# Kernel optimization log

Measured on AMD Instinct MI355X. Metric: run time of the kernel, lower is better.

## Reference

```python
import jax, jax.numpy as jnp
import numpy as np

NUM_HEADS = 8
WINDOW_SIZE = 4
DIM = 384


def setup_inputs() -> dict:
    key = jax.random.key(0)
    k_x, k_qkv, k_pw, k_pb = jax.random.split(key, 4)
    B, N, C = 8, 16384, DIM
    x = jax.random.normal(k_x, (B, N, C), dtype=jnp.float32)
    # torch nn.Linear weights are [out_features, in_features]
    W_qkv = jax.random.normal(k_qkv, (3 * C, C), dtype=jnp.float32) * (1.0 / np.sqrt(C))
    W_proj = jax.random.normal(k_pw, (C, C), dtype=jnp.float32) * (1.0 / np.sqrt(C))
    b_proj = jax.random.normal(k_pb, (C,), dtype=jnp.float32) * 0.01
    return {"x": x, "W_qkv": W_qkv, "W_proj": W_proj, "b_proj": b_proj}


def reference(x, W_qkv, W_proj, b_proj):
    B, N, C = x.shape
    H = int(round(N ** 0.5))
    W = H
    ws = WINDOW_SIZE
    nh = NUM_HEADS
    hd = C // nh
    scale = hd ** -0.5
    hw, ww = H // ws, W // ws

    qkv = x @ W_qkv.T  # [B, N, 3C]
    qkv = qkv.reshape(B, N, 3, nh, hd)
    qkv = jnp.transpose(qkv, (2, 0, 3, 1, 4))  # [3, B, nh, N, hd]
    q, k, v = qkv[0], qkv[1], qkv[2]

    def to_windows(t):
        # [B, nh, N, hd] -> [B, nh, n_windows, ws*ws, hd]
        t = t.reshape(B, nh, hw, ws, ww, ws, hd)
        t = jnp.transpose(t, (0, 1, 2, 4, 3, 5, 6))
        return t.reshape(B, nh, hw * ww, ws * ws, hd)

    q, k, v = to_windows(q), to_windows(k), to_windows(v)

    attn = jnp.einsum('bhwqd,bhwkd->bhwqk', q, k) * scale
    attn = jax.nn.softmax(attn, axis=-1)
    out = jnp.einsum('bhwqk,bhwkd->bhwqd', attn, v)

    # windows back to [B, N, C]
    out = out.reshape(B, nh, hw, ww, ws, ws, hd)
    out = jnp.transpose(out, (0, 1, 2, 4, 3, 5, 6)).reshape(B, nh, N, hd)
    out = jnp.transpose(out, (0, 2, 1, 3)).reshape(B, N, C)

    out = out @ W_proj.T + b_proj
    return out
```

## Files before the change

### kernel.cpp

```cpp
#include <hip/hip_runtime.h>
#include <hip/hip_bf16.h>
#include <cstdint>

#define ASPACE(n) __attribute__((address_space(n)))

typedef short bf16x8 __attribute__((ext_vector_type(8)));
typedef float f32x4 __attribute__((ext_vector_type(4)));

__device__ __forceinline__ unsigned short f2bf(float f) {
  uint32_t u = __float_as_uint(f);
  u += 0x7fffu + ((u >> 16) & 1u);
  return (unsigned short)(u >> 16);
}
__device__ __forceinline__ float bf2f(unsigned short h) {
  return __uint_as_float(((uint32_t)h) << 16);
}

__global__ __launch_bounds__(256) void conv_f32_bf16(const float4* __restrict__ src,
                                                     ushort4* __restrict__ dst, int n4) {
  int i = blockIdx.x * blockDim.x + threadIdx.x;
  int stride = gridDim.x * blockDim.x;
  for (; i < n4; i += stride) {
    float4 v = src[i];
    ushort4 o;
    o.x = f2bf(v.x); o.y = f2bf(v.y); o.z = f2bf(v.z); o.w = f2bf(v.w);
    dst[i] = o;
  }
}

__device__ __forceinline__ void gload16(const unsigned short* g, unsigned short* l) {
  __builtin_amdgcn_global_load_lds((const ASPACE(1) void*)g, (ASPACE(3) void*)l, 16, 0, 0);
}

template <int OUT_MODE>
__global__ __launch_bounds__(256, 3) void gemm_bt(const unsigned short* __restrict__ A,
                                                  const unsigned short* __restrict__ B,
                                                  void* __restrict__ Cout,
                                                  const float* __restrict__ bias,
                                                  int M, int N, int K) {
  __shared__ unsigned short As[2][128 * 32];
  __shared__ unsigned short Bs[2][192 * 32];

  const int tid  = threadIdx.x;
  const int lane = tid & 63;
  const int wave = tid >> 6;
  const int wr = wave >> 1;
  const int wc = wave & 1;

  const int nwg = gridDim.x;
  const int swz = (blockIdx.x & 7) * (nwg >> 3) + (blockIdx.x >> 3);
  const int ntn = N / 192;
  const int bn0 = (swz % ntn) * 192;
  const int bm0 = (swz / ntn) << 7;

  const unsigned short* Abase = A + (size_t)bm0 * K;
  const unsigned short* Bbase = B + (size_t)bn0 * K;

  const unsigned short* gA[2];
  const unsigned short* gB[3];
  unsigned short* lA[2];
  unsigned short* lB[3];
#pragma unroll
  for (int i = 0; i < 2; ++i) {
    const int c = i * 256 + tid;
    const int r = c >> 2;
    const int gc = (c & 3) ^ ((r >> 1) & 3);
    gA[i] = Abase + (size_t)r * K + gc * 8;
    lA[i] = (unsigned short*)As + (i * 256 + wave * 64) * 8;
  }
#pragma unroll
  for (int i = 0; i < 3; ++i) {
    const int c = i * 256 + tid;
    const int r = c >> 2;
    const int gc = (c & 3) ^ ((r >> 1) & 3);
    gB[i] = Bbase + (size_t)r * K + gc * 8;
    lB[i] = (unsigned short*)Bs + (i * 256 + wave * 64) * 8;
  }
  const int abufoff = 128 * 32;
  const int bbufoff = 192 * 32;

  const int fr = lane & 15;
  const int hi = lane >> 4;
  int afo[4], bfo[6];
#pragma unroll
  for (int m = 0; m < 4; ++m) {
    const int row = wr * 64 + m * 16 + fr;
    afo[m] = row * 32 + ((hi ^ ((row >> 1) & 3)) * 8);
  }
#pragma unroll
  for (int n = 0; n < 6; ++n) {
    const int row = wc * 96 + n * 16 + fr;
    bfo[n] = row * 32 + ((hi ^ ((row >> 1) & 3)) * 8);
  }

  f32x4 acc[4][6];
#pragma unroll
  for (int m = 0; m < 4; ++m)
#pragma unroll
    for (int n = 0; n < 6; ++n) {
      f32x4 z = {0.f, 0.f, 0.f, 0.f};
      acc[m][n] = z;
    }

  const int NT = K >> 5;

#pragma unroll
  for (int i = 0; i < 2; ++i) gload16(gA[i], lA[i]);
#pragma unroll
  for (int i = 0; i < 3; ++i) gload16(gB[i], lB[i]);
  __syncthreads();

  int cur = 0;
  for (int t = 0; t < NT; ++t) {
    if (t + 1 < NT) {
      const int nb = cur ^ 1;
      const int k0 = (t + 1) << 5;
#pragma unroll
      for (int i = 0; i < 2; ++i) gload16(gA[i] + k0, lA[i] + nb * abufoff);
#pragma unroll
      for (int i = 0; i < 3; ++i) gload16(gB[i] + k0, lB[i] + nb * bbufoff);
    }
    {
      const unsigned short* Ab = (const unsigned short*)As + cur * abufoff;
      const unsigned short* Bb = (const unsigned short*)Bs + cur * bbufoff;
      bf16x8 af[4], bfv[6];
#pragma unroll
      for (int m = 0; m < 4; ++m) af[m] = *(const bf16x8*)(Ab + afo[m]);
#pragma unroll
      for (int n = 0; n < 6; ++n) bfv[n] = *(const bf16x8*)(Bb + bfo[n]);
#pragma unroll
      for (int m = 0; m < 4; ++m)
#pragma unroll
        for (int n = 0; n < 6; ++n)
          acc[m][n] = __builtin_amdgcn_mfma_f32_16x16x32_bf16(af[m], bfv[n], acc[m][n], 0, 0, 0);
    }
    __syncthreads();
    cur ^= 1;
  }

  const int rq = hi * 4;
  if (OUT_MODE == 1) {
    float* C = (float*)Cout;
#pragma unroll
    for (int m = 0; m < 4; ++m) {
#pragma unroll
      for (int n = 0; n < 6; ++n) {
        const int col = bn0 + wc * 96 + n * 16 + fr;
        const float bv = bias[col];
#pragma unroll
        for (int r = 0; r < 4; ++r) {
          const int row = bm0 + wr * 64 + m * 16 + rq + r;
          C[(size_t)row * N + col] = acc[m][n][r] + bv;
        }
      }
    }
  } else {
    unsigned short* C = (unsigned short*)Cout;
#pragma unroll
    for (int m = 0; m < 4; ++m) {
#pragma unroll
      for (int n = 0; n < 6; ++n) {
        const int col = bn0 + wc * 96 + n * 16 + fr;
        const int pl = col / 48;
        const int d  = col - pl * 48;
        unsigned short* base = C + ((size_t)pl * M + bm0 + wr * 64 + m * 16 + rq) * 48 + d;
#pragma unroll
        for (int r = 0; r < 4; ++r)
          base[(size_t)r * 48] = f2bf(acc[m][n][r]);
      }
    }
  }
}

#define PADV 24
#define PADP 24
#define MTOK 131072
__global__ __launch_bounds__(256) void win_attn(const unsigned short* __restrict__ qkv,
                                                unsigned short* __restrict__ aout) {
  __shared__ unsigned short lds[4][48 * PADV + 16 * PADP];
  const int tid = threadIdx.x;
  const int wave = tid >> 6, lane = tid & 63;
  const int wg = blockIdx.x * 4 + wave;
  const int h = wg & 7;
  const int bw = wg >> 3;
  const int w = bw & 1023, b = bw >> 10;
  const int wy = w >> 5, wx = w & 31;

  unsigned short* Vt = lds[wave];
  unsigned short* P  = lds[wave] + 48 * PADV;

  const int lg = lane >> 4;
  const int lr = lane & 15;

  const int gtok = b * 16384 + (wy * 4 + (lr >> 2)) * 128 + wx * 4 + (lr & 3);
  const size_t qb = ((size_t)h * MTOK + gtok) * 48;
  const size_t kb = ((size_t)(8 + h) * MTOK + gtok) * 48;
  const size_t vb = ((size_t)(16 + h) * MTOK + gtok) * 48;

  bf16x8 aq0, bk0;
  bf16x8 aq1 = {0, 0, 0, 0, 0, 0, 0, 0};
  bf16x8 bk1 = {0, 0, 0, 0, 0, 0, 0, 0};
  aq0 = *(const bf16x8*)(qkv + qb + lg * 8);
  bk0 = *(const bf16x8*)(qkv + kb + lg * 8);
  if (lg < 2) {
    aq1 = *(const bf16x8*)(qkv + qb + 32 + lg * 8);
    bk1 = *(const bf16x8*)(qkv + kb + 32 + lg * 8);
  }

  {
    bf16x8 v = *(const bf16x8*)(qkv + vb + lg * 8);
#pragma unroll
    for (int i = 0; i < 8; ++i) Vt[(lg * 8 + i) * PADV + lr] = (unsigned short)v[i];
    if (lane < 32) {
      bf16x8 v2 = *(const bf16x8*)(qkv + vb + 32 + lg * 8);
#pragma unroll
      for (int i = 0; i < 8; ++i) Vt[((4 + lg) * 8 + i) * PADV + lr] = (unsigned short)v2[i];
    }
  }

  f32x4 s = {0.f, 0.f, 0.f, 0.f};
  s = __builtin_amdgcn_mfma_f32_16x16x32_bf16(aq0, bk0, s, 0, 0, 0);
  s = __builtin_amdgcn_mfma_f32_16x16x32_bf16(aq1, bk1, s, 0, 0, 0);

  const float scale = 0.14433756729740643f;
  float p[4];
#pragma unroll
  for (int r = 0; r < 4; ++r) {
    float x = s[r] * scale;
    float m = x;
    m = fmaxf(m, __shfl_xor(m, 1));
    m = fmaxf(m, __shfl_xor(m, 2));
    m = fmaxf(m, __shfl_xor(m, 4));
    m = fmaxf(m, __shfl_xor(m, 8));
    float e = __expf(x - m);
    float t = e;
    t += __shfl_xor(t, 1);
    t += __shfl_xor(t, 2);
    t += __shfl_xor(t, 4);
    t += __shfl_xor(t, 8);
    p[r] = e / t;
  }
#pragma unroll
  for (int r = 0; r < 4; ++r) P[(lg * 4 + r) * PADP + lr] = f2bf(p[r]);

  __syncthreads();

  bf16x8 ap = {0, 0, 0, 0, 0, 0, 0, 0};
  if (lg < 2) ap = *(const bf16x8*)(P + lr * PADP + lg * 8);

  f32x4 o[3];
#pragma unroll
  for (int c = 0; c < 3; ++c) {
    bf16x8 bv = {0, 0, 0, 0, 0, 0, 0, 0};
    if (lg < 2) bv = *(const bf16x8*)(Vt + (c * 16 + lr) * PADV + lg * 8);
    f32x4 z = {0.f, 0.f, 0.f, 0.f};
    o[c] = __builtin_amdgcn_mfma_f32_16x16x32_bf16(ap, bv, z, 0, 0, 0);
  }

#pragma unroll
  for (int r = 0; r < 4; ++r) {
    const int qi = lg * 4 + r;
    const int nq = (wy * 4 + (qi >> 2)) * 128 + wx * 4 + (qi & 3);
    const size_t obase = ((size_t)(b * 16384 + nq)) * 384 + h * 48;
#pragma unroll
    for (int c = 0; c < 3; ++c)
      aout[obase + c * 16 + lr] = f2bf(o[c][r]);
  }
}

extern "C" void kernel_launch(void* const* d_in, const int* in_sizes, int n_in,
                              void* d_out, int out_size, void* d_ws, size_t ws_size,
                              hipStream_t stream) {
  const float* x      = (const float*)d_in[0];
  const float* W_qkv  = (const float*)d_in[1];
  const float* W_proj = (const float*)d_in[2];
  const float* b_proj = (const float*)d_in[3];
  float* out = (float*)d_out;

  const int Bb = 8, Nn = 16384, Cc = 384;
  const int M = Bb * Nn;
  const int threeC = 3 * Cc;

  char* ws = (char*)d_ws;
  unsigned short* qkv_bf   = (unsigned short*)ws;
  unsigned short* xa_bf    = (unsigned short*)(ws + (size_t)M * threeC * 2);
  unsigned short* wqkv_bf  = (unsigned short*)(ws + (size_t)M * threeC * 2 + (size_t)M * Cc * 2);
  unsigned short* wproj_bf = wqkv_bf + threeC * Cc;

  conv_f32_bf16<<<2048, 256, 0, stream>>>((const float4*)x, (ushort4*)xa_bf, M * Cc / 4);
  conv_f32_bf16<<<432, 256, 0, stream>>>((const float4*)W_qkv, (ushort4*)wqkv_bf, threeC * Cc / 4);
  conv_f32_bf16<<<144, 256, 0, stream>>>((const float4*)W_proj, (ushort4*)wproj_bf, Cc * Cc / 4);

  gemm_bt<0><<<(M / 128) * (threeC / 192), 256, 0, stream>>>(xa_bf, wqkv_bf, qkv_bf, nullptr,
                                                             M, threeC, Cc);

  win_attn<<<Bb * 8 * 1024 / 4, 256, 0, stream>>>(qkv_bf, xa_bf);

  gemm_bt<1><<<(M / 128) * (Cc / 192), 256, 0, stream>>>(xa_bf, wproj_bf, out, b_proj,
                                                         M, Cc, Cc);
}
```

Before: 421.9 us.

## Fuse window attention with output projection GEMM via LDS-resident attention tile

```diff
diff --git a/kernel.cpp b/kernel.cpp
--- a/kernel.cpp
+++ b/kernel.cpp
@@ -32,12 +32,10 @@
   __builtin_amdgcn_global_load_lds((const ASPACE(1) void*)g, (ASPACE(3) void*)l, 16, 0, 0);
 }
 
-template <int OUT_MODE>
-__global__ __launch_bounds__(256, 3) void gemm_bt(const unsigned short* __restrict__ A,
-                                                  const unsigned short* __restrict__ B,
-                                                  void* __restrict__ Cout,
-                                                  const float* __restrict__ bias,
-                                                  int M, int N, int K) {
+__global__ __launch_bounds__(256, 3) void gemm_qkv(const unsigned short* __restrict__ A,
+                                                   const unsigned short* __restrict__ B,
+                                                   unsigned short* __restrict__ C,
+                                                   int M, int N, int K) {
   __shared__ unsigned short As[2][128 * 32];
   __shared__ unsigned short Bs[2][192 * 32];
 
@@ -139,132 +137,203 @@
   }
 
   const int rq = hi * 4;
-  if (OUT_MODE == 1) {
-    float* C = (float*)Cout;
-#pragma unroll
-    for (int m = 0; m < 4; ++m) {
-#pragma unroll
-      for (int n = 0; n < 6; ++n) {
-        const int col = bn0 + wc * 96 + n * 16 + fr;
-        const float bv = bias[col];
-#pragma unroll
-        for (int r = 0; r < 4; ++r) {
-          const int row = bm0 + wr * 64 + m * 16 + rq + r;
-          C[(size_t)row * N + col] = acc[m][n][r] + bv;
-        }
-      }
-    }
-  } else {
-    unsigned short* C = (unsigned short*)Cout;
-#pragma unroll
-    for (int m = 0; m < 4; ++m) {
-#pragma unroll
-      for (int n = 0; n < 6; ++n) {
-        const int col = bn0 + wc * 96 + n * 16 + fr;
-        const int pl = col / 48;
-        const int d  = col - pl * 48;
-        unsigned short* base = C + ((size_t)pl * M + bm0 + wr * 64 + m * 16 + rq) * 48 + d;
-#pragma unroll
-        for (int r = 0; r < 4; ++r)
-          base[(size_t)r * 48] = f2bf(acc[m][n][r]);
-      }
-    }
-  }
-}
-
-#define PADV 24
-#define PADP 24
+#pragma unroll
+  for (int m = 0; m < 4; ++m) {
+#pragma unroll
+    for (int n = 0; n < 6; ++n) {
+      const int col = bn0 + wc * 96 + n * 16 + fr;
+      const int pl = col / 48;
+      const int d  = col - pl * 48;
+      unsigned short* base = C + ((size_t)pl * M + bm0 + wr * 64 + m * 16 + rq) * 48 + d;
+#pragma unroll
+      for (int r = 0; r < 4; ++r)
+        base[(size_t)r * 48] = f2bf(acc[m][n][r]);
+    }
+  }
+}
+
 #define MTOK 131072
-__global__ __launch_bounds__(256) void win_attn(const unsigned short* __restrict__ qkv,
-                                                unsigned short* __restrict__ aout) {
-  __shared__ unsigned short lds[4][48 * PADV + 16 * PADP];
-  const int tid = threadIdx.x;
-  const int wave = tid >> 6, lane = tid & 63;
-  const int wg = blockIdx.x * 4 + wave;
-  const int h = wg & 7;
-  const int bw = wg >> 3;
-  const int w = bw & 1023, b = bw >> 10;
-  const int wy = w >> 5, wx = w & 31;
-
-  unsigned short* Vt = lds[wave];
-  unsigned short* P  = lds[wave] + 48 * PADV;
+#define ASTR 392
+__global__ __launch_bounds__(512, 2) void fused_attn_proj(const unsigned short* __restrict__ qkv,
+                                                          const unsigned short* __restrict__ Wp,
+                                                          const float* __restrict__ bias,
+                                                          float* __restrict__ out) {
+  __shared__ unsigned short lds[50176 + 24576];
+  unsigned short* attn = lds;
+  unsigned short* BsS  = lds + 50176;
+
+  const int tid = threadIdx.x, lane = tid & 63, wave = tid >> 6;
+  const int nwg = gridDim.x;
+  const int swz = (blockIdx.x & 7) * (nwg >> 3) + (blockIdx.x >> 3);
+  const int b = swz >> 7, g2 = swz & 127;
+  const int yb = g2 >> 2, xb = g2 & 3;
+  const int imgbase = b * 16384;
 
   const int lg = lane >> 4;
   const int lr = lane & 15;
 
-  const int gtok = b * 16384 + (wy * 4 + (lr >> 2)) * 128 + wx * 4 + (lr & 3);
-  const size_t qb = ((size_t)h * MTOK + gtok) * 48;
-  const size_t kb = ((size_t)(8 + h) * MTOK + gtok) * 48;
-  const size_t vb = ((size_t)(16 + h) * MTOK + gtok) * 48;
-
-  bf16x8 aq0, bk0;
-  bf16x8 aq1 = {0, 0, 0, 0, 0, 0, 0, 0};
-  bf16x8 bk1 = {0, 0, 0, 0, 0, 0, 0, 0};
-  aq0 = *(const bf16x8*)(qkv + qb + lg * 8);
-  bk0 = *(const bf16x8*)(qkv + kb + lg * 8);
-  if (lg < 2) {
-    aq1 = *(const bf16x8*)(qkv + qb + 32 + lg * 8);
-    bk1 = *(const bf16x8*)(qkv + kb + 32 + lg * 8);
-  }
-
   {
-    bf16x8 v = *(const bf16x8*)(qkv + vb + lg * 8);
-#pragma unroll
-    for (int i = 0; i < 8; ++i) Vt[(lg * 8 + i) * PADV + lr] = (unsigned short)v[i];
-    if (lane < 32) {
-      bf16x8 v2 = *(const bf16x8*)(qkv + vb + 32 + lg * 8);
-#pragma unroll
-      for (int i = 0; i < 8; ++i) Vt[((4 + lg) * 8 + i) * PADV + lr] = (unsigned short)v2[i];
-    }
-  }
-
-  f32x4 s = {0.f, 0.f, 0.f, 0.f};
-  s = __builtin_amdgcn_mfma_f32_16x16x32_bf16(aq0, bk0, s, 0, 0, 0);
-  s = __builtin_amdgcn_mfma_f32_16x16x32_bf16(aq1, bk1, s, 0, 0, 0);
-
-  const float scale = 0.14433756729740643f;
-  float p[4];
-#pragma unroll
-  for (int r = 0; r < 4; ++r) {
-    float x = s[r] * scale;
-    float m = x;
-    m = fmaxf(m, __shfl_xor(m, 1));
-    m = fmaxf(m, __shfl_xor(m, 2));
-    m = fmaxf(m, __shfl_xor(m, 4));
-    m = fmaxf(m, __shfl_xor(m, 8));
-    float e = __expf(x - m);
-    float t = e;
-    t += __shfl_xor(t, 1);
-    t += __shfl_xor(t, 2);
-    t += __shfl_xor(t, 4);
-    t += __shfl_xor(t, 8);
-    p[r] = e / t;
-  }
-#pragma unroll
-  for (int r = 0; r < 4; ++r) P[(lg * 4 + r) * PADP + lr] = f2bf(p[r]);
-
+    unsigned short* Vt = BsS + wave * 1536;
+    unsigned short* P  = Vt + 48 * 24;
+    const int gtok = imgbase + (yb * 4 + (lr >> 2)) * 128 + xb * 32 + wave * 4 + (lr & 3);
+
+    for (int h = 0; h < 8; ++h) {
+      const size_t qb = ((size_t)h * MTOK + gtok) * 48;
+      const size_t kb = ((size_t)(8 + h) * MTOK + gtok) * 48;
+      const size_t vb = ((size_t)(16 + h) * MTOK + gtok) * 48;
+
+      bf16x8 aq0 = *(const bf16x8*)(qkv + qb + lg * 8);
+      bf16x8 bk0 = *(const bf16x8*)(qkv + kb + lg * 8);
+      bf16x8 aq1 = {0, 0, 0, 0, 0, 0, 0, 0};
+      bf16x8 bk1 = {0, 0, 0, 0, 0, 0, 0, 0};
+      if (lg < 2) {
+        aq1 = *(const bf16x8*)(qkv + qb + 32 + lg * 8);
+        bk1 = *(const bf16x8*)(qkv + kb + 32 + lg * 8);
+      }
+      {
+        bf16x8 v = *(const bf16x8*)(qkv + vb + lg * 8);
+#pragma unroll
+        for (int i = 0; i < 8; ++i) Vt[(lg * 8 + i) * 24 + lr] = (unsigned short)v[i];
+        if (lane < 32) {
+          bf16x8 v2 = *(const bf16x8*)(qkv + vb + 32 + lg * 8);
+#pragma unroll
+          for (int i = 0; i < 8; ++i) Vt[((4 + lg) * 8 + i) * 24 + lr] = (unsigned short)v2[i];
+        }
+      }
+
+      f32x4 s = {0.f, 0.f, 0.f, 0.f};
+      s = __builtin_amdgcn_mfma_f32_16x16x32_bf16(aq0, bk0, s, 0, 0, 0);
+      s = __builtin_amdgcn_mfma_f32_16x16x32_bf16(aq1, bk1, s, 0, 0, 0);
+
+      const float scale = 0.14433756729740643f;
+      float p[4];
+#pragma unroll
+      for (int r = 0; r < 4; ++r) {
+        float xv = s[r] * scale;
+        float m = xv;
+        m = fmaxf(m, __shfl_xor(m, 1));
+        m = fmaxf(m, __shfl_xor(m, 2));
+        m = fmaxf(m, __shfl_xor(m, 4));
+        m = fmaxf(m, __shfl_xor(m, 8));
+        float e = __expf(xv - m);
+        float tt = e;
+        tt += __shfl_xor(tt, 1);
+        tt += __shfl_xor(tt, 2);
+        tt += __shfl_xor(tt, 4);
+        tt += __shfl_xor(tt, 8);
+        p[r] = e / tt;
+      }
+#pragma unroll
+      for (int r = 0; r < 4; ++r) P[(lg * 4 + r) * 24 + lr] = f2bf(p[r]);
+
+      __syncthreads();
+
+      bf16x8 ap = {0, 0, 0, 0, 0, 0, 0, 0};
+      if (lg < 2) ap = *(const bf16x8*)(P + lr * 24 + lg * 8);
+
+      f32x4 o[3];
+#pragma unroll
+      for (int c = 0; c < 3; ++c) {
+        bf16x8 bv = {0, 0, 0, 0, 0, 0, 0, 0};
+        if (lg < 2) bv = *(const bf16x8*)(Vt + (c * 16 + lr) * 24 + lg * 8);
+        f32x4 z = {0.f, 0.f, 0.f, 0.f};
+        o[c] = __builtin_amdgcn_mfma_f32_16x16x32_bf16(ap, bv, z, 0, 0, 0);
+      }
+
+#pragma unroll
+      for (int r = 0; r < 4; ++r) {
+        const int qi = lg * 4 + r;
+        const int lq = (qi >> 2) * 32 + wave * 4 + (qi & 3);
+#pragma unroll
+        for (int c = 0; c < 3; ++c)
+          attn[lq * ASTR + h * 48 + c * 16 + lr] = f2bf(o[c][r]);
+      }
+      __syncthreads();
+    }
+  }
+
+  const int fr = lane & 15;
+  const int hi = lane >> 4;
+  const int wr = wave >> 1;
+  const int wc = wave & 1;
+
+  const unsigned short* gB[3];
+  unsigned short* lB[3];
+#pragma unroll
+  for (int i = 0; i < 3; ++i) {
+    const int c = i * 512 + tid;
+    const int r = c >> 2;
+    const int gc = (c & 3) ^ ((r >> 1) & 3);
+    gB[i] = Wp + (size_t)r * 384 + gc * 8;
+    lB[i] = BsS + (i * 512 + wave * 64) * 8;
+  }
+  const int bbufoff = 384 * 32;
+
+  int afo[2], bfo[12];
+#pragma unroll
+  for (int mf = 0; mf < 2; ++mf) {
+    const int row = wr * 32 + mf * 16 + fr;
+    afo[mf] = row * ASTR;
+  }
+#pragma unroll
+  for (int nf = 0; nf < 12; ++nf) {
+    const int row = wc * 192 + nf * 16 + fr;
+    bfo[nf] = row * 32 + ((hi ^ ((row >> 1) & 3)) * 8);
+  }
+
+  f32x4 acc[2][12];
+#pragma unroll
+  for (int mf = 0; mf < 2; ++mf)
+#pragma unroll
+    for (int nf = 0; nf < 12; ++nf) {
+      f32x4 z = {0.f, 0.f, 0.f, 0.f};
+      acc[mf][nf] = z;
+    }
+
+#pragma unroll
+  for (int i = 0; i < 3; ++i) gload16(gB[i], lB[i]);
   __syncthreads();
 
-  bf16x8 ap = {0, 0, 0, 0, 0, 0, 0, 0};
-  if (lg < 2) ap = *(const bf16x8*)(P + lr * PADP + lg * 8);
-
-  f32x4 o[3];
-#pragma unroll
-  for (int c = 0; c < 3; ++c) {
-    bf16x8 bv = {0, 0, 0, 0, 0, 0, 0, 0};
-    if (lg < 2) bv = *(const bf16x8*)(Vt + (c * 16 + lr) * PADV + lg * 8);
-    f32x4 z = {0.f, 0.f, 0.f, 0.f};
-    o[c] = __builtin_amdgcn_mfma_f32_16x16x32_bf16(ap, bv, z, 0, 0, 0);
-  }
-
-#pragma unroll
-  for (int r = 0; r < 4; ++r) {
-    const int qi = lg * 4 + r;
-    const int nq = (wy * 4 + (qi >> 2)) * 128 + wx * 4 + (qi & 3);
-    const size_t obase = ((size_t)(b * 16384 + nq)) * 384 + h * 48;
-#pragma unroll
-    for (int c = 0; c < 3; ++c)
-      aout[obase + c * 16 + lr] = f2bf(o[c][r]);
+  int cur = 0;
+  for (int t = 0; t < 12; ++t) {
+    if (t + 1 < 12) {
+      const int nb = cur ^ 1;
+      const int k0 = (t + 1) << 5;
+#pragma unroll
+      for (int i = 0; i < 3; ++i) gload16(gB[i] + k0, lB[i] + nb * bbufoff);
+    }
+    {
+      const unsigned short* Bb = BsS + cur * bbufoff;
+      bf16x8 af[2], bfv[12];
+#pragma unroll
+      for (int mf = 0; mf < 2; ++mf)
+        af[mf] = *(const bf16x8*)(attn + afo[mf] + t * 32 + hi * 8);
+#pragma unroll
+      for (int nf = 0; nf < 12; ++nf) bfv[nf] = *(const bf16x8*)(Bb + bfo[nf]);
+#pragma unroll
+      for (int mf = 0; mf < 2; ++mf)
+#pragma unroll
+        for (int nf = 0; nf < 12; ++nf)
+          acc[mf][nf] = __builtin_amdgcn_mfma_f32_16x16x32_bf16(af[mf], bfv[nf], acc[mf][nf], 0, 0, 0);
+    }
+    __syncthreads();
+    cur ^= 1;
+  }
+
+  const int rq = hi * 4;
+#pragma unroll
+  for (int mf = 0; mf < 2; ++mf) {
+#pragma unroll
+    for (int nf = 0; nf < 12; ++nf) {
+      const int col = wc * 192 + nf * 16 + fr;
+      const float bv = bias[col];
+#pragma unroll
+      for (int r = 0; r < 4; ++r) {
+        const int l = wr * 32 + mf * 16 + rq + r;
+        const int gtok = imgbase + (yb * 4 + (l >> 5)) * 128 + xb * 32 + (l & 31);
+        out[(size_t)gtok * 384 + col] = acc[mf][nf][r] + bv;
+      }
+    }
   }
 }
 
@@ -283,19 +352,16 @@
 
   char* ws = (char*)d_ws;
   unsigned short* qkv_bf   = (unsigned short*)ws;
-  unsigned short* xa_bf    = (unsigned short*)(ws + (size_t)M * threeC * 2);
+  unsigned short* x_bf     = (unsigned short*)(ws + (size_t)M * threeC * 2);
   unsigned short* wqkv_bf  = (unsigned short*)(ws + (size_t)M * threeC * 2 + (size_t)M * Cc * 2);
   unsigned short* wproj_bf = wqkv_bf + threeC * Cc;
 
-  conv_f32_bf16<<<2048, 256, 0, stream>>>((const float4*)x, (ushort4*)xa_bf, M * Cc / 4);
+  conv_f32_bf16<<<2048, 256, 0, stream>>>((const float4*)x, (ushort4*)x_bf, M * Cc / 4);
   conv_f32_bf16<<<432, 256, 0, stream>>>((const float4*)W_qkv, (ushort4*)wqkv_bf, threeC * Cc / 4);
   conv_f32_bf16<<<144, 256, 0, stream>>>((const float4*)W_proj, (ushort4*)wproj_bf, Cc * Cc / 4);
 
-  gemm_bt<0><<<(M / 128) * (threeC / 192), 256, 0, stream>>>(xa_bf, wqkv_bf, qkv_bf, nullptr,
-                                                             M, threeC, Cc);
-
-  win_attn<<<Bb * 8 * 1024 / 4, 256, 0, stream>>>(qkv_bf, xa_bf);
-
-  gemm_bt<1><<<(M / 128) * (Cc / 192), 256, 0, stream>>>(xa_bf, wproj_bf, out, b_proj,
-                                                         M, Cc, Cc);
-}
+  gemm_qkv<<<(M / 128) * (threeC / 192), 256, 0, stream>>>(x_bf, wqkv_bf, qkv_bf,
+                                                           M, threeC, Cc);
+
+  fused_attn_proj<<<M / 128, 512, 0, stream>>>(qkv_bf, wproj_bf, b_proj, out);
+}
```

After: 407.2 us. 1.04x faster.
